# Kernel tuning notes

Hardware: AMD Instinct MI355X
Metric: run time of the kernel (lower is better)

The kernel has to match this reference:

```python
import jax, jax.numpy as jnp
import numpy as np

IN_CH = 256
NUM_CLASSES = 1
CONF_THR = 0.3
NMS_IOU = 0.2
ANCHOR_SIZES = (32.0, 64.0, 128.0)
ASPECTS = (0.5, 1.0, 2.0)
NUM_ANCHORS = len(ANCHOR_SIZES) * len(ASPECTS)  # 9
K_CAND = 1024   # top-score candidates fed to NMS per image
MAX_DET = 100   # max_output_size in source
BN_EPS = 1e-5


def _anchors():
    a = [[s * r / 224.0, s / r / 224.0] for s in ANCHOR_SIZES for r in ASPECTS]
    return jnp.asarray(a, jnp.float32)  # [A, 2] (w, h)


def _conv(x, w, b, pad):
    y = jax.lax.conv_general_dilated(x, w, (1, 1), [(pad, pad), (pad, pad)],
                                     dimension_numbers=('NCHW', 'OIHW', 'NCHW'))
    return y + b[None, :, None, None]


def _bn(x, g, b, m, v):
    inv = jax.lax.rsqrt(v + BN_EPS)
    return (x - m[None, :, None, None]) * (g * inv)[None, :, None, None] + b[None, :, None, None]


def _corners(b):
    return (b[..., 0] - b[..., 2] / 2, b[..., 1] - b[..., 3] / 2,
            b[..., 0] + b[..., 2] / 2, b[..., 1] + b[..., 3] / 2)


def _iou_one(box, boxes):
    # box: [4] cxcywh, boxes: [K,4] -> iou [K]
    ax1, ay1, ax2, ay2 = _corners(box)
    bx1, by1, bx2, by2 = _corners(boxes)
    iw = jnp.maximum(jnp.minimum(ax2, bx2) - jnp.maximum(ax1, bx1), 0.0)
    ih = jnp.maximum(jnp.minimum(ay2, by2) - jnp.maximum(ay1, by1), 0.0)
    inter = iw * ih
    union = (ax2 - ax1) * (ay2 - ay1) + (bx2 - bx1) * (by2 - by1) - inter
    return inter / (union + 1e-16)


def _nms(boxes, scores):
    # boxes [K,4], scores [K] -> kept boxes padded to [MAX_DET,4]
    s0 = jnp.where(scores > CONF_THR, scores, -1.0)

    def body(i, carry):
        s, out = carry
        j = jnp.argmax(s)
        ok = s[j] > 0.0
        box = boxes[j]
        iou = _iou_one(box, boxes)
        s_new = jnp.where(iou > NMS_IOU, -1.0, s).at[j].set(-1.0)
        s = jnp.where(ok, s_new, s)
        out = out.at[i].set(jnp.where(ok, box, jnp.zeros_like(box)))
        return s, out

    _, out = jax.lax.fori_loop(0, MAX_DET, body,
                               (s0, jnp.zeros((MAX_DET, 4), boxes.dtype)))
    return out


def _forward(features, w1, b1, g1, be1, m1, v1, w2, b2, g2, be2, m2, v2, wo, bo):
    x = jax.nn.relu(_bn(_conv(features, w1, b1, 1), g1, be1, m1, v1))
    x = jax.nn.relu(_bn(_conv(x, w2, b2, 1), g2, be2, m2, v2))
    p = _conv(x, wo, bo, 0)                      # [B, A*(5+C), H, W]
    B, _, H, W = p.shape
    p = p.reshape(B, NUM_ANCHORS, 5 + NUM_CLASSES, H, W).transpose(0, 3, 4, 1, 2)  # [B,H,W,A,5+C]
    obj = jax.nn.sigmoid(p[..., 4])
    anch = _anchors()
    gx = jnp.arange(W, dtype=p.dtype)[None, :, None]
    gy = jnp.arange(H, dtype=p.dtype)[:, None, None]
    px = (jax.nn.sigmoid(p[..., 0]) + gx) / W
    py = (jax.nn.sigmoid(p[..., 1]) + gy) / H
    pw = jnp.exp(p[..., 2]) * anch[:, 0]
    ph = jnp.exp(p[..., 3]) * anch[:, 1]
    boxes = jnp.stack([px, py, pw, ph], -1).reshape(B, -1, 4)
    if NUM_CLASSES > 1:
        scores = obj * jax.nn.sigmoid(p[..., 5:]).max(-1)
    else:
        scores = obj
    scores = scores.reshape(B, -1)

    def per_image(bx, sc):
        top_s, idx = jax.lax.top_k(sc, K_CAND)
        return _nms(bx[idx], top_s)

    return jax.vmap(per_image)(boxes, scores)    # [B, MAX_DET, 4]


def setup_inputs() -> dict:
    key = jax.random.key(0)
    ks = jax.random.split(key, 16)
    B = 32
    c1, c2 = IN_CH // 2, IN_CH // 4
    oc = NUM_ANCHORS * (5 + NUM_CLASSES)
    return {
        'features': jax.random.normal(ks[0], (B, IN_CH, 56, 56), jnp.float32),
        'w1': jax.random.normal(ks[1], (c1, IN_CH, 3, 3), jnp.float32) * 0.02,
        'b1': jax.random.normal(ks[2], (c1,), jnp.float32) * 0.02,
        'g1': 1.0 + 0.1 * jax.random.normal(ks[3], (c1,), jnp.float32),
        'be1': 0.1 * jax.random.normal(ks[4], (c1,), jnp.float32),
        'm1': 0.1 * jax.random.normal(ks[5], (c1,), jnp.float32),
        'v1': jax.random.uniform(ks[6], (c1,), jnp.float32, 0.5, 1.5),
        'w2': jax.random.normal(ks[7], (c2, c1, 3, 3), jnp.float32) * 0.03,
        'b2': jax.random.normal(ks[8], (c2,), jnp.float32) * 0.02,
        'g2': 1.0 + 0.1 * jax.random.normal(ks[9], (c2,), jnp.float32),
        'be2': 0.1 * jax.random.normal(ks[10], (c2,), jnp.float32),
        'm2': 0.1 * jax.random.normal(ks[11], (c2,), jnp.float32),
        'v2': jax.random.uniform(ks[12], (c2,), jnp.float32, 0.5, 1.5),
        'wo': jax.random.normal(ks[13], (oc, c2, 1, 1), jnp.float32) * 0.1,
        'bo': jax.random.normal(ks[14], (oc,), jnp.float32) * 0.05,
    }


def reference(features, w1, b1, g1, be1, m1, v1, w2, b2, g2, be2, m2, v2, wo, bo):
    return _forward(features, w1, b1, g1, be1, m1, v1, w2, b2, g2, be2, m2, v2, wo, bo)
```

## Files before the change

kernel.cpp:

```cpp
#include <hip/hip_runtime.h>
#include <math.h>
#include <stdint.h>

constexpr int BB   = 32;
constexpr int HW   = 3136;
constexpr int C0   = 256, C1 = 128, C2 = 64;
constexpr int NA   = 9;
constexpr int NCAND = HW * NA;
constexpr int KSEL  = 1024;
constexpr int MAXDET = 100;

typedef _Float16 half8 __attribute__((ext_vector_type(8)));
typedef _Float16 half4v __attribute__((ext_vector_type(4)));
typedef float    f32x4  __attribute__((ext_vector_type(4)));
typedef float    f32x16 __attribute__((ext_vector_type(16)));

__device__ __forceinline__ void g2l16(const void* g, void* l) {
    auto gp = reinterpret_cast<const __attribute__((address_space(1))) char*>(
        reinterpret_cast<uintptr_t>(g));
    auto lp = reinterpret_cast<__attribute__((address_space(3))) char*>(
        reinterpret_cast<uintptr_t>(l));
    __builtin_amdgcn_global_load_lds(gp, lp, 16, 0, 0);
}

__global__ void bn_prep2(const float* g1, const float* be1, const float* m1,
                         const float* v1, const float* cb1,
                         const float* g2, const float* be2, const float* m2,
                         const float* v2, const float* cb2,
                         float* scl1, float* tb1, float* scl2, float* tb2) {
    int i = threadIdx.x;
    if (i < C1) {
        float inv = 1.f / sqrtf(v1[i] + 1e-5f);
        float s = g1[i] * inv;
        scl1[i] = s;
        tb1[i] = be1[i] + (cb1[i] - m1[i]) * s;
    }
    if (i < C2) {
        float inv = 1.f / sqrtf(v2[i] + 1e-5f);
        float s = g2[i] * inv;
        scl2[i] = s;
        tb2[i] = be2[i] + (cb2[i] - m2[i]) * s;
    }
}

__device__ __forceinline__ void reorder_one(const float* w, _Float16* wc,
                                            int i, int CIN, int COUT) {
    int K = CIN * 9;
    int ci  = i & 31;
    int row = (i >> 5) % (2 * COUT);
    int ch  = (i >> 5) / (2 * COUT);
    int pl  = row / COUT;
    int oc  = row - pl * COUT;
    int cg = ch / 9, r = ch - cg * 9;
    int cin = cg * 32 + ci;
    float v = w[oc * K + cin * 9 + r];
    _Float16 h = (_Float16)v;
    wc[i] = pl ? (_Float16)(v - (float)h) : h;
}

__global__ void reorder_w_both(const float* __restrict__ w1, _Float16* __restrict__ w1c,
                               const float* __restrict__ w2, _Float16* __restrict__ w2c) {
    constexpr int N1 = 2 * C1 * C0 * 9;
    constexpr int N2 = 2 * C2 * C1 * 9;
    int i = blockIdx.x * 256 + threadIdx.x;
    if (i < N1) reorder_one(w1, w1c, i, C0, C1);
    else if (i < N1 + N2) reorder_one(w2, w2c, i - N1, C1, C2);
}

__global__ __launch_bounds__(256) void nchw_to_nhwc_split(
    const float* __restrict__ in, _Float16* __restrict__ hi, _Float16* __restrict__ lo)
{
    __shared__ float tile[64 * 68];
    const int pt = blockIdx.x * 64, ct = blockIdx.y * 64, b = blockIdx.z;
    const int t = threadIdx.x;
    const int r0 = t >> 4, cidx = (t & 15) * 4;
#pragma unroll
    for (int rr = 0; rr < 64; rr += 16) {
        int r = rr + r0;
        const float* src = in + ((size_t)(b * 256 + ct + r)) * HW + pt + cidx;
        float4 v = *(const float4*)src;
        float* d = &tile[r * 68 + cidx];
        d[0] = v.x; d[1] = v.y; d[2] = v.z; d[3] = v.w;
    }
    __syncthreads();
    const int p = t >> 2, c0 = (t & 3) * 16;
    size_t obase = ((size_t)(b * HW + pt + p)) * 256 + ct + c0;
    half8 h0, h1, l0, l1;
#pragma unroll
    for (int j = 0; j < 16; ++j) {
        float v = tile[(c0 + j) * 68 + p];
        _Float16 hh = (_Float16)v;
        _Float16 ll = (_Float16)(v - (float)hh);
        if (j < 8) { h0[j] = hh; l0[j] = ll; }
        else       { h1[j - 8] = hh; l1[j - 8] = ll; }
    }
    *(half8*)(hi + obase)     = h0;
    *(half8*)(hi + obase + 8) = h1;
    *(half8*)(lo + obase)     = l0;
    *(half8*)(lo + obase + 8) = l1;
}

template <int CIN, int COUT, int MINW, bool NHWC_OUT>
__global__ __launch_bounds__(256, MINW) void conv3x3_v12(
    const _Float16* __restrict__ xhi,
    const _Float16* __restrict__ xlo,
    const _Float16* __restrict__ wc,
    const _Float16* __restrict__ zbuf,
    const float* __restrict__ scl, const float* __restrict__ tb,
    _Float16* __restrict__ ohi,
    _Float16* __restrict__ olo,
    float* __restrict__ onchw)
{
    constexpr int K       = CIN * 9;
    constexpr int NCH     = K / 32;
    constexpr int WROWS   = 2 * COUT;
    constexpr int CHALVES = WROWS * 32;
    constexpr int WI      = WROWS / 64;
    constexpr int PI      = 2;
    constexpr int WOC     = COUT / 64;

    __shared__ __align__(16) _Float16 SP[128 * 64];
    __shared__ __align__(16) _Float16 SW[WROWS * 32];

    const int bid = blockIdx.x;
    const int swz = (bid & 7) * (gridDim.x >> 3) + (bid >> 3);
    const int b = swz / 25;
    const int pixBase = (swz - b * 25) * 128;
    const int bHW = b * HW;

    const int t = threadIdx.x, l = t & 63, w = t >> 6;

    const int cpix = (l & 7) ^ ((l >> 3) & 7);
    const int ppl = cpix >> 2, pq = cpix & 3;
    const _Float16* xsp = ppl ? xlo : xhi;
    int py[4], px[4];
    const _Float16* pbase[4];
#pragma unroll
    for (int i = 0; i < 4; ++i) {
        int p = w * 32 + i * 8 + (l >> 3);
        int pix = pixBase + p;
        py[i] = pix / 56; px[i] = pix - py[i] * 56;
        pbase[i] = xsp + (size_t)(bHW + pix) * CIN + pq * 8;
    }
    const _Float16* wbase = wc + ((size_t)(w * (WI * 16) + (l >> 2))) * 32 + (l & 3) * 8;

    const int wid = t >> 6;
    const int wp = wid & 1, wo = wid >> 1;
    const int lc = l & 31, lk = l >> 5;

    f32x16 acc[PI][WOC];
#pragma unroll
    for (int pi = 0; pi < PI; ++pi)
#pragma unroll
        for (int oi = 0; oi < WOC; ++oi) acc[pi][oi] = (f32x16)0.f;

    auto stage = [&](int ch) {
        int cg = ch / 9, r = ch - cg * 9;
        int ky = r / 3;
        int dy = ky - 1, dx = (r - ky * 3) - 1;
        int off = (dy * 56 + dx) * CIN + cg * 32;
#pragma unroll
        for (int i = 0; i < 4; ++i) {
            bool v = ((unsigned)(py[i] + dy) < 56u) && ((unsigned)(px[i] + dx) < 56u);
            const void* src = v ? (const void*)(pbase[i] + off) : (const void*)zbuf;
            g2l16(src, (void*)&SP[w * 2048 + i * 512]);
        }
        const _Float16* wsrc = wbase + (size_t)ch * CHALVES;
#pragma unroll
        for (int j = 0; j < WI; ++j)
            g2l16((const void*)(wsrc + j * 512), (void*)&SW[(w * WI + j) * 512]);
    };

    auto compute = [&]() {
#pragma unroll
        for (int ks = 0; ks < 2; ++ks) {
            half8 pb[PI][2];
#pragma unroll
            for (int pi = 0; pi < PI; ++pi) {
                int prw = wp * (PI * 32) + pi * 32 + lc;
                int key = prw & 7;
#pragma unroll
                for (int pl2 = 0; pl2 < 2; ++pl2) {
                    int c = pl2 * 4 + ks * 2 + lk;
                    pb[pi][pl2] = *(const half8*)&SP[prw * 64 + ((c ^ key) << 3)];
                }
            }
            half8 wa[WOC][2];
#pragma unroll
            for (int oi = 0; oi < WOC; ++oi)
#pragma unroll
                for (int pl2 = 0; pl2 < 2; ++pl2) {
                    int row = pl2 * COUT + wo * (WOC * 32) + oi * 32 + lc;
                    int c = ks * 2 + lk;
                    wa[oi][pl2] = *(const half8*)&SW[row * 32 + (c << 3)];
                }
#pragma unroll
            for (int pi = 0; pi < PI; ++pi)
#pragma unroll
                for (int oi = 0; oi < WOC; ++oi) {
                    acc[pi][oi] = __builtin_amdgcn_mfma_f32_32x32x16_f16(wa[oi][0], pb[pi][0], acc[pi][oi], 0, 0, 0);
                    acc[pi][oi] = __builtin_amdgcn_mfma_f32_32x32x16_f16(wa[oi][0], pb[pi][1], acc[pi][oi], 0, 0, 0);
                    acc[pi][oi] = __builtin_amdgcn_mfma_f32_32x32x16_f16(wa[oi][1], pb[pi][0], acc[pi][oi], 0, 0, 0);
                }
        }
    };

    for (int ch = 0; ch < NCH; ++ch) {
        stage(ch);
        __syncthreads();
        compute();
        __syncthreads();
    }

#pragma unroll
    for (int pi = 0; pi < PI; ++pi) {
        const int pix = pixBase + wp * (PI * 32) + pi * 32 + lc;
        if (pix < HW) {
#pragma unroll
            for (int oi = 0; oi < WOC; ++oi) {
#pragma unroll
                for (int g = 0; g < 4; ++g) {
                    const int oc0 = wo * (WOC * 32) + oi * 32 + 8 * g + 4 * lk;
                    f32x4 s4 = *(const f32x4*)(scl + oc0);
                    f32x4 t4 = *(const f32x4*)(tb + oc0);
                    if constexpr (NHWC_OUT) {
                        half4v hh, ll;
#pragma unroll
                        for (int m2 = 0; m2 < 4; ++m2) {
                            float val = fmaxf(acc[pi][oi][g * 4 + m2] * s4[m2] + t4[m2], 0.f);
                            _Float16 h = (_Float16)val;
                            hh[m2] = h;
                            ll[m2] = (_Float16)(val - (float)h);
                        }
                        size_t o = ((size_t)(bHW + pix)) * COUT + oc0;
                        *(half4v*)(ohi + o) = hh;
                        *(half4v*)(olo + o) = ll;
                    } else {
#pragma unroll
                        for (int m2 = 0; m2 < 4; ++m2) {
                            float val = fmaxf(acc[pi][oi][g * 4 + m2] * s4[m2] + t4[m2], 0.f);
                            onchw[((size_t)(b * COUT + oc0 + m2)) * HW + pix] = val;
                        }
                    }
                }
            }
        }
    }
}

__global__ __launch_bounds__(256) void conv1x1_decode(
    const float* __restrict__ x2, const float* __restrict__ wo,
    const float* __restrict__ bo,
    float* __restrict__ boxes, float* __restrict__ scores)
{
    __shared__ float ws[64 * 56];
    for (int i = threadIdx.x; i < 54 * 64; i += 256) {
        int oc = i % 54, c = i / 54;
        ws[c * 56 + oc] = wo[oc * 64 + c];
    }
    __syncthreads();

    int u = blockIdx.x * 256 + threadIdx.x;
    int a = u % 9;
    int rest = u / 9;
    int quad = rest % 784;
    int b = rest / 784;
    int pix0 = quad * 4;
    int y = pix0 / 56;
    int x0 = pix0 - y * 56;

    const float* xb = x2 + (size_t)b * 64 * HW + pix0;
    float acc[5][4];
#pragma unroll
    for (int j = 0; j < 5; ++j)
#pragma unroll
        for (int p = 0; p < 4; ++p) acc[j][p] = 0.f;

#pragma unroll 8
    for (int c = 0; c < 64; ++c) {
        float4 xv = *(const float4*)(xb + c * HW);
#pragma unroll
        for (int j = 0; j < 5; ++j) {
            float w = ws[c * 56 + a * 6 + j];
            acc[j][0] += w * xv.x;
            acc[j][1] += w * xv.y;
            acc[j][2] += w * xv.z;
            acc[j][3] += w * xv.w;
        }
    }

    int si = a / 3, ri = a - si * 3;
    float sv = (float)(32 << si);
    float rv = 0.5f * (float)(1 << ri);
    float aw = (sv * rv) / 224.f;
    float ah = (sv / rv) / 224.f;
    float bo0 = bo[a * 6 + 0], bo1 = bo[a * 6 + 1], bo2 = bo[a * 6 + 2];
    float bo3 = bo[a * 6 + 3], bo4 = bo[a * 6 + 4];

#pragma unroll
    for (int p = 0; p < 4; ++p) {
        float p0 = acc[0][p] + bo0;
        float p1 = acc[1][p] + bo1;
        float p2 = acc[2][p] + bo2;
        float p3 = acc[3][p] + bo3;
        float p4 = acc[4][p] + bo4;
        float sx = 1.f / (1.f + expf(-p0));
        float sy = 1.f / (1.f + expf(-p1));
        float pxc = (sx + (float)(x0 + p)) / 56.f;
        float pyc = (sy + (float)y) / 56.f;
        float pw = expf(p2) * aw;
        float ph = expf(p3) * ah;
        float sc = 1.f / (1.f + expf(-p4));
        int n = (y * 56 + x0 + p) * 9 + a;
        float4 bx; bx.x = pxc; bx.y = pyc; bx.z = pw; bx.w = ph;
        *(float4*)&boxes[((size_t)b * NCAND + n) * 4] = bx;
        scores[(size_t)b * NCAND + n] = sc;
    }
}

__device__ __forceinline__ unsigned fkey(float f) {
    unsigned u = __float_as_uint(f);
    return (u & 0x80000000u) ? ~u : (u | 0x80000000u);
}

__global__ __launch_bounds__(1024) void topk_select(
    const float* __restrict__ scores, const float* __restrict__ boxes,
    float* __restrict__ cbox, float* __restrict__ csc, int* __restrict__ cidx)
{
    const int b = blockIdx.x, t = threadIdx.x;
    const float* sp = scores + (size_t)b * NCAND;
    const int lane = t & 63, w = t >> 6;

    __shared__ unsigned hist[256];
    __shared__ unsigned wsum[16];
    __shared__ unsigned s_sel, s_need, s_tot0, s_tot1;

    unsigned prefix = 0, maskSo = 0;
    int need = KSEL;

    for (int round = 0; round < 4; ++round) {
        int shift = 24 - round * 8;
        if (t < 256) hist[t] = 0;
        __syncthreads();
        for (int i = t; i < NCAND; i += 1024) {
            unsigned u = fkey(sp[i]);
            if ((u & maskSo) == prefix) atomicAdd(&hist[(u >> shift) & 255], 1u);
        }
        __syncthreads();
        if (t == 0) {
            int rem = need;
            unsigned sel = 0;
            for (int v = 255; v >= 0; --v) {
                int c = (int)hist[v];
                if (c >= rem) { sel = (unsigned)v; break; }
                rem -= c;
            }
            s_sel = sel; s_need = (unsigned)rem;
        }
        __syncthreads();
        prefix |= (s_sel << shift);
        maskSo |= (0xFFu << shift);
        need = (int)s_need;
        __syncthreads();
    }

    const unsigned cutoff = prefix;
    const unsigned needT = (unsigned)need;
    unsigned outBase = 0, tieBase = 0;
    const unsigned long long mlt = (1ull << lane) - 1ull;

    for (int c0 = 0; c0 < NCAND; c0 += 1024) {
        int i = c0 + t;
        bool valid = i < NCAND;
        float sc = valid ? sp[i] : 0.f;
        unsigned u = valid ? fkey(sc) : 0u;
        bool gt = valid && (u > cutoff);
        bool eq = valid && (u == cutoff);

        unsigned long long balE = __ballot(eq);
        unsigned lpE = (unsigned)__popcll(balE & mlt);
        if (lane == 0) wsum[w] = (unsigned)__popcll(balE);
        __syncthreads();
        if (t == 0) {
            unsigned run = 0;
            for (int k = 0; k < 16; ++k) { unsigned x = wsum[k]; wsum[k] = run; run += x; }
            s_tot1 = run;
        }
        __syncthreads();
        unsigned tieRank = tieBase + wsum[w] + lpE;
        bool take = gt || (eq && tieRank < needT);
        __syncthreads();

        unsigned long long balT = __ballot(take);
        unsigned lpT = (unsigned)__popcll(balT & mlt);
        if (lane == 0) wsum[w] = (unsigned)__popcll(balT);
        __syncthreads();
        if (t == 0) {
            unsigned run = 0;
            for (int k = 0; k < 16; ++k) { unsigned x = wsum[k]; wsum[k] = run; run += x; }
            s_tot0 = run;
        }
        __syncthreads();
        unsigned pos = outBase + wsum[w] + lpT;
        if (take) {
            float4 bx = *(const float4*)&boxes[((size_t)b * NCAND + i) * 4];
            *(float4*)&cbox[((size_t)b * KSEL + pos) * 4] = bx;
            csc[(size_t)b * KSEL + pos] = sc;
            cidx[(size_t)b * KSEL + pos] = i;
        }
        tieBase += s_tot1;
        outBase += s_tot0;
        __syncthreads();
    }
}

__global__ __launch_bounds__(64) void nms_wave(
    const float* __restrict__ cbox, const float* __restrict__ csc,
    const int* __restrict__ cidx, float* __restrict__ out)
{
    const int b = blockIdx.x, l = threadIdx.x;
    float cx[16], cy[16], w_[16], h_[16], s[16];
    int id[16];
#pragma unroll
    for (int j = 0; j < 16; ++j) {
        int ci = (b << 10) + (j << 6) + l;
        float4 bb = *(const float4*)&cbox[(size_t)ci * 4];
        float sc = csc[ci];
        cx[j] = bb.x; cy[j] = bb.y; w_[j] = bb.z; h_[j] = bb.w;
        s[j] = sc > 0.3f ? sc : -1.f;
        id[j] = cidx[ci];
    }
    float* ob = out + (size_t)b * MAXDET * 4;

    for (int it = 0; it < MAXDET; ++it) {
        float bs = s[0]; int bi = id[0];
        float bcx = cx[0], bcy = cy[0], bw = w_[0], bh = h_[0];
#pragma unroll
        for (int j = 1; j < 16; ++j) {
            bool tk = (s[j] > bs) || (s[j] == bs && id[j] < bi);
            if (tk) { bs = s[j]; bi = id[j]; bcx = cx[j]; bcy = cy[j]; bw = w_[j]; bh = h_[j]; }
        }
#pragma unroll
        for (int m2 = 1; m2 < 64; m2 <<= 1) {
            float os = __shfl_xor(bs, m2); int oi = __shfl_xor(bi, m2);
            float ox = __shfl_xor(bcx, m2), oy = __shfl_xor(bcy, m2);
            float ow = __shfl_xor(bw, m2), oh2 = __shfl_xor(bh, m2);
            bool tk = (os > bs) || (os == bs && oi < bi);
            if (tk) { bs = os; bi = oi; bcx = ox; bcy = oy; bw = ow; bh = oh2; }
        }
        if (bs <= 0.f) {
            for (int q = it * 4 + l; q < MAXDET * 4; q += 64) ob[q] = 0.f;
            break;
        }
        if (l == 0) {
            float4 o; o.x = bcx; o.y = bcy; o.z = bw; o.w = bh;
            *(float4*)&ob[it * 4] = o;
        }
        float wx1 = bcx - bw / 2.f, wy1 = bcy - bh / 2.f;
        float wx2 = bcx + bw / 2.f, wy2 = bcy + bh / 2.f;
        float war = (wx2 - wx1) * (wy2 - wy1);
#pragma unroll
        for (int j = 0; j < 16; ++j) {
            float jx1 = cx[j] - w_[j] / 2.f, jy1 = cy[j] - h_[j] / 2.f;
            float jx2 = cx[j] + w_[j] / 2.f, jy2 = cy[j] + h_[j] / 2.f;
            float iw = fminf(wx2, jx2) - fmaxf(wx1, jx1); iw = fmaxf(iw, 0.f);
            float ih = fminf(wy2, jy2) - fmaxf(wy1, jy1); ih = fmaxf(ih, 0.f);
            float inter = iw * ih;
            float jar = (jx2 - jx1) * (jy2 - jy1);
            float uni = war + jar - inter;
            if (inter / (uni + 1e-16f) > 0.2f) s[j] = -1.f;
        }
    }
}

extern "C" void kernel_launch(void* const* d_in, const int* in_sizes, int n_in,
                              void* d_out, int out_size, void* d_ws, size_t ws_size,
                              hipStream_t stream)
{
    const float* features = (const float*)d_in[0];
    const float* w1 = (const float*)d_in[1];
    const float* b1 = (const float*)d_in[2];
    const float* g1 = (const float*)d_in[3];
    const float* be1 = (const float*)d_in[4];
    const float* m1 = (const float*)d_in[5];
    const float* v1 = (const float*)d_in[6];
    const float* w2 = (const float*)d_in[7];
    const float* b2 = (const float*)d_in[8];
    const float* g2 = (const float*)d_in[9];
    const float* be2 = (const float*)d_in[10];
    const float* m2 = (const float*)d_in[11];
    const float* v2 = (const float*)d_in[12];
    const float* wo = (const float*)d_in[13];
    const float* bo = (const float*)d_in[14];

    char* ws = (char*)d_ws;
    size_t off = 0;
    auto alloc = [&](size_t bytes) {
        char* p = ws + off;
        off += (bytes + 255) / 256 * 256;
        return p;
    };

    _Float16* zbuf = (_Float16*)alloc(256);
    _Float16* w1c = (_Float16*)alloc((size_t)2 * C1 * 2304 * 2);
    _Float16* w2c = (_Float16*)alloc((size_t)2 * C2 * 1152 * 2);
    float* scl1 = (float*)alloc(C1 * 4);
    float* tb1  = (float*)alloc(C1 * 4);
    float* scl2 = (float*)alloc(C2 * 4);
    float* tb2  = (float*)alloc(C2 * 4);

    const size_t planeF = (size_t)BB * HW * C0 * 2;
    char* regB = alloc(2 * planeF);
    _Float16* fhi = (_Float16*)regB;
    _Float16* flo = (_Float16*)(regB + planeF);

    const size_t planeX1 = (size_t)BB * HW * C1 * 2;
    char* regC = alloc(2 * planeX1);
    _Float16* x1hi = (_Float16*)regC;
    _Float16* x1lo = (_Float16*)(regC + planeX1);

    float* x2     = (float*)regB;
    float* boxes  = (float*)(regB + 25690112);
    float* scores = (float*)(regB + 25690112 + 14450688);
    float* cbox = (float*)regC;
    float* csc  = (float*)(regC + 524288);
    int*   cidx = (int*)(regC + 524288 + 131072);

    hipMemsetAsync(zbuf, 0, 256, stream);
    bn_prep2<<<1, 256, 0, stream>>>(g1, be1, m1, v1, b1, g2, be2, m2, v2, b2,
                                    scl1, tb1, scl2, tb2);
    {
        int total = 2 * C1 * 2304 + 2 * C2 * 1152;
        reorder_w_both<<<(total + 255) / 256, 256, 0, stream>>>(w1, w1c, w2, w2c);
    }

    nchw_to_nhwc_split<<<dim3(49, 4, BB), 256, 0, stream>>>(features, fhi, flo);

    conv3x3_v12<C0, C1, 4, true><<<800, 256, 0, stream>>>(
        fhi, flo, w1c, zbuf, scl1, tb1, x1hi, x1lo, nullptr);
    conv3x3_v12<C1, C2, 4, false><<<800, 256, 0, stream>>>(
        x1hi, x1lo, w2c, zbuf, scl2, tb2, nullptr, nullptr, x2);

    conv1x1_decode<<<(BB * 784 * NA) / 256, 256, 0, stream>>>(x2, wo, bo, boxes, scores);

    topk_select<<<BB, 1024, 0, stream>>>(scores, boxes, cbox, csc, cidx);
    nms_wave<<<BB, 64, 0, stream>>>(cbox, csc, cidx, (float*)d_out);
}
```

Before: 646.2 us.

## Use 3-round 11/10/10-bit radix select with two-level histogram scan

The top-k radix select now makes three passes over the candidate scores instead of four, using 11, 10 and 10 bit digits. It assumes the sign bit of the key is set, which holds for non-negative sigmoid scores. The serial scan of the larger histogram is replaced by a parallel sum over groups of 32 bins followed by a short scan inside the chosen group. The intent is to save one full read of the scores per image, at the cost of more LDS atomics contention spread over larger histograms.

Measured after the change: 608.9 us. 5.8% less time.

```diff
diff --git a/kernel.cpp b/kernel.cpp
--- a/kernel.cpp
+++ b/kernel.cpp
@@ -331,35 +331,52 @@
     const float* sp = scores + (size_t)b * NCAND;
     const int lane = t & 63, w = t >> 6;
 
-    __shared__ unsigned hist[256];
+    __shared__ unsigned hist[2048];
+    __shared__ unsigned gsum[64];
     __shared__ unsigned wsum[16];
     __shared__ unsigned s_sel, s_need, s_tot0, s_tot1;
 
-    unsigned prefix = 0, maskSo = 0;
+    unsigned prefix = 0x80000000u, maskSo = 0x80000000u;
     int need = KSEL;
 
-    for (int round = 0; round < 4; ++round) {
-        int shift = 24 - round * 8;
-        if (t < 256) hist[t] = 0;
+    for (int round = 0; round < 3; ++round) {
+        const int shift = (round == 0) ? 20 : (round == 1 ? 10 : 0);
+        const unsigned bmask = (round == 0) ? 2047u : 1023u;
+        const int ngroups = (round == 0) ? 64 : 32;
+
+        hist[t] = 0;
+        if (round == 0) hist[t + 1024] = 0;
         __syncthreads();
         for (int i = t; i < NCAND; i += 1024) {
             unsigned u = fkey(sp[i]);
-            if ((u & maskSo) == prefix) atomicAdd(&hist[(u >> shift) & 255], 1u);
+            if ((u & maskSo) == prefix) atomicAdd(&hist[(u >> shift) & bmask], 1u);
+        }
+        __syncthreads();
+        if (t < ngroups) {
+            unsigned s = 0;
+#pragma unroll 8
+            for (int k = 0; k < 32; ++k) s += hist[t * 32 + k];
+            gsum[t] = s;
         }
         __syncthreads();
         if (t == 0) {
             int rem = need;
-            unsigned sel = 0;
-            for (int v = 255; v >= 0; --v) {
+            int g = ngroups - 1;
+            for (;; --g) {
+                if ((int)gsum[g] >= rem || g == 0) break;
+                rem -= (int)gsum[g];
+            }
+            unsigned sel = (unsigned)(g * 32);
+            for (int v = g * 32 + 31; v >= g * 32; --v) {
                 int c = (int)hist[v];
-                if (c >= rem) { sel = (unsigned)v; break; }
+                if (c >= rem || v == g * 32) { sel = (unsigned)v; break; }
                 rem -= c;
             }
             s_sel = sel; s_need = (unsigned)rem;
         }
         __syncthreads();
         prefix |= (s_sel << shift);
-        maskSo |= (0xFFu << shift);
+        maskSo |= (bmask << shift);
         need = (int)s_need;
         __syncthreads();
     }
```
